# Kernel optimization log

Measured on AMD Instinct MI355X. Metric: run time of the kernel, lower is better.

The kernel has to match this reference:

```python
import jax, jax.numpy as jnp
import numpy as np

E, C, F, K = 8, 768, 3072, 2  # NUM_EXPERTS, EMBED_DIM, FFN_DIM, TOP_K


def setup_inputs() -> dict:
    key = jax.random.key(0)
    k0, k1, k2, k3 = jax.random.split(key, 4)
    B, T = 8, 2048
    return {
        "x": jax.random.normal(k0, (B, T, C), jnp.float32),
        "router_w": jax.random.normal(k1, (E, C), jnp.float32) * 0.02,
        "w1": jax.random.normal(k2, (E, C, F), jnp.float32) * 0.02,
        "b1": jnp.zeros((E, F), jnp.float32),
        "w2": jax.random.normal(k3, (E, F, C), jnp.float32) * 0.02,
        "b2": jnp.zeros((E, C), jnp.float32),
    }


def reference(x, router_w, w1, b1, w2, b2):
    # Dropout is inference-mode identity (eval). GELU is torch's exact (erf) variant.
    B, T, Cc = x.shape
    flat = x.reshape(-1, Cc)                                   # [N, C]
    logits = flat @ router_w.T                                 # [N, E]
    probs = jax.nn.softmax(logits.astype(jnp.float32), axis=-1)
    top_w, top_i = jax.lax.top_k(probs, K)                     # [N, K]
    top_w = (top_w / top_w.sum(-1, keepdims=True)).astype(x.dtype)
    out = jnp.zeros_like(flat)
    for e in range(E):
        # per-token combine weight for expert e (0 if token not routed to e)
        w_e = jnp.sum(top_w * (top_i == e), axis=-1)[:, None]  # [N, 1]
        h = jax.nn.gelu(flat @ w1[e] + b1[e], approximate=False)  # [N, F]
        out = out + w_e * (h @ w2[e] + b2[e])
    return out.reshape(B, T, Cc)
```

## Files before the change

### kernel.cpp

```cpp
#include <hip/hip_runtime.h>
#include <hip/hip_bf16.h>

#define NTOK 16384
#define CDIM 768
#define FDIM 3072
#define NEXP 8
#define NSLOT 32768
#define HBLK 128
#define MAXT256 135

typedef __attribute__((ext_vector_type(8))) short bf16x8;
typedef __attribute__((ext_vector_type(4))) float f32x4;
typedef __attribute__((ext_vector_type(8))) unsigned short u16x8;

__device__ __forceinline__ unsigned short f2bf(float f) {
  unsigned int u = __float_as_uint(f);
  u += 0x7FFFu + ((u >> 16) & 1u);
  return (unsigned short)(u >> 16);
}
__device__ __forceinline__ float bf2f(unsigned short h) {
  return __uint_as_float((unsigned int)h << 16);
}

__device__ __forceinline__ float fast_gelu(float x) {
  float x2 = x * x;
  float z = x * __builtin_fmaf(0.070565402f, x2, 1.5975981f);
  float s = __builtin_amdgcn_rcpf(1.0f + __expf(-z));
  return x * s;
}

__device__ __forceinline__ void async16(const void* g, void* l) {
  __builtin_amdgcn_global_load_lds(
      (const __attribute__((address_space(1))) unsigned int*)g,
      (__attribute__((address_space(3))) unsigned int*)l, 16, 0, 0);
}

#define BARRIER() asm volatile("s_barrier" ::: "memory")
#define LGK0()    asm volatile("s_waitcnt lgkmcnt(0)" ::: "memory")
#define VMC(n)    asm volatile("s_waitcnt vmcnt(" #n ")" ::: "memory")

__global__ __launch_bounds__(256)
void k_transpose(const float* __restrict__ src, unsigned short* __restrict__ dst,
                 int R, int Cc)
{
  __shared__ float tle[32][33];
  int e = blockIdx.z;
  int c0 = blockIdx.x * 32, r0 = blockIdx.y * 32;
  int tx = threadIdx.x & 31, ty = threadIdx.x >> 5;
  const float* s = src + (size_t)e * R * Cc;
  unsigned short* d = dst + (size_t)e * R * Cc;
#pragma unroll
  for (int i = 0; i < 4; ++i)
    tle[ty + i * 8][tx] = s[(size_t)(r0 + ty + i * 8) * Cc + c0 + tx];
  __syncthreads();
#pragma unroll
  for (int i = 0; i < 4; ++i)
    d[(size_t)(c0 + ty + i * 8) * R + r0 + tx] = f2bf(tle[tx][ty + i * 8]);
}

__global__ __launch_bounds__(256)
void k_router(const float* __restrict__ x, const float* __restrict__ rw,
              int* __restrict__ tk_e, float* __restrict__ tk_w)
{
  __shared__ float srw[NEXP * CDIM];
  int tid = threadIdx.x;
#pragma unroll
  for (int i = 0; i < (NEXP * CDIM / 4) / 256; ++i)
    ((float4*)srw)[tid + i * 256] = ((const float4*)rw)[tid + i * 256];
  __syncthreads();
  int lane = tid & 63, wid = tid >> 6;
  int t = blockIdx.x * 4 + wid;
  float a[NEXP];
#pragma unroll
  for (int e = 0; e < NEXP; ++e) a[e] = 0.f;
  const float* xr = x + (size_t)t * CDIM;
#pragma unroll
  for (int c = 0; c < CDIM / 64; ++c) {
    float xv = xr[c * 64 + lane];
#pragma unroll
    for (int e = 0; e < NEXP; ++e) a[e] += xv * srw[e * CDIM + c * 64 + lane];
  }
#pragma unroll
  for (int e = 0; e < NEXP; ++e) {
#pragma unroll
    for (int off = 32; off; off >>= 1) a[e] += __shfl_xor(a[e], off);
  }
  if (lane == 0) {
    int i0 = 0; float l0 = a[0];
#pragma unroll
    for (int e = 1; e < NEXP; ++e) if (a[e] > l0) { l0 = a[e]; i0 = e; }
    int i1 = -1; float l1 = -1e30f;
#pragma unroll
    for (int e = 0; e < NEXP; ++e) if (e != i0 && a[e] > l1) { l1 = a[e]; i1 = e; }
    float w0 = 1.f / (1.f + expf(l1 - l0));
    tk_e[2 * t] = i0;     tk_e[2 * t + 1] = i1;
    tk_w[2 * t] = w0;     tk_w[2 * t + 1] = 1.f - w0;
  }
}

__global__ __launch_bounds__(256)
void k_hist(const int* __restrict__ tk_e, int* __restrict__ blockhist)
{
  __shared__ int h[NEXP];
  int tid = threadIdx.x;
  if (tid < NEXP) h[tid] = 0;
  __syncthreads();
  int e = tk_e[blockIdx.x * 256 + tid];
  atomicAdd(&h[e], 1);
  __syncthreads();
  if (tid < NEXP) blockhist[blockIdx.x * NEXP + tid] = h[tid];
}

__global__ __launch_bounds__(512)
void k_scan2(const int* __restrict__ blockhist, int* __restrict__ counts,
             int* __restrict__ offsets, int* __restrict__ tp,
             int* __restrict__ blockbase)
{
  __shared__ int ltot[NEXP];
  __shared__ int loff[NEXP + 1];
  int tid = threadIdx.x;
  int lane = tid & 63, e = tid >> 6;
  int o0 = blockhist[lane * NEXP + e];
  int o1 = blockhist[(64 + lane) * NEXP + e];
  int h0 = o0, h1 = o1;
#pragma unroll
  for (int d = 1; d < 64; d <<= 1) { int v = __shfl_up(h0, d); if (lane >= d) h0 += v; }
  int s0 = __shfl(h0, 63);
#pragma unroll
  for (int d = 1; d < 64; d <<= 1) { int v = __shfl_up(h1, d); if (lane >= d) h1 += v; }
  h1 += s0;
  if (lane == 63) ltot[e] = h1;
  __syncthreads();
  if (tid == 0) {
    loff[0] = 0;
    int tpv = 0; tp[0] = 0;
    for (int k = 0; k < NEXP; ++k) {
      loff[k + 1] = loff[k] + ltot[k];
      counts[k] = ltot[k];
      offsets[k] = loff[k];
      tpv += (ltot[k] + 255) / 256;
      tp[k + 1] = tpv;
    }
    offsets[NEXP] = loff[NEXP];
  }
  __syncthreads();
  int base = loff[e];
  blockbase[lane * NEXP + e]        = base + h0 - o0;
  blockbase[(64 + lane) * NEXP + e] = base + h1 - o1;
}

__global__ __launch_bounds__(256)
void k_assign_gather(const float* __restrict__ x, const int* __restrict__ tk_e,
                     const float* __restrict__ tk_w,
                     const int* __restrict__ blockbase,
                     int* __restrict__ tok2slot, float* __restrict__ slot_w,
                     unsigned short* __restrict__ Xg)
{
  __shared__ int eh[256];
  __shared__ int sslot[256];
  int b = blockIdx.x, tid = threadIdx.x;
  int pick = b * 256 + tid;
  int e = tk_e[pick];
  eh[tid] = e;
  __syncthreads();
  int rank = 0;
  for (int j = 0; j < tid; ++j) rank += (eh[j] == e);
  int slot = blockbase[b * NEXP + e] + rank;
  sslot[tid] = slot;
  tok2slot[pick] = slot;
  slot_w[slot] = tk_w[pick];
  __syncthreads();
  int lane = tid & 63, wid = tid >> 6;
  for (int p = wid * 64; p < wid * 64 + 64; ++p) {
    int token = (b * 256 + p) >> 1;
    int s = sslot[p];
    const float4* src = (const float4*)(x + (size_t)token * CDIM);
    ushort4* dst = (ushort4*)(Xg + (size_t)s * CDIM);
#pragma unroll
    for (int i = 0; i < 3; ++i) {
      float4 v = src[i * 64 + lane];
      ushort4 hh;
      hh.x = f2bf(v.x); hh.y = f2bf(v.y); hh.z = f2bf(v.z); hh.w = f2bf(v.w);
      dst[i * 64 + lane] = hh;
    }
  }
}

__global__ __launch_bounds__(512, 2)
void k_gemm1(const unsigned short* __restrict__ A, int lda,
             const unsigned short* __restrict__ B, int ldb, long sB,
             const int* __restrict__ counts,
             const int* __restrict__ offsets, const int* __restrict__ tp,
             int t0, const float* __restrict__ bias, int biasStride,
             unsigned short* __restrict__ Hout, int ldh, int gx, int nwg)
{
  constexpr int KI = CDIM / 128;
  __shared__ __align__(16) char lds[131072];

  int orig = blockIdx.y * gx + blockIdx.x;
  int q = nwg >> 3, r = nwg & 7;
  int xcd = orig & 7, jj = orig >> 3;
  int wgid = (xcd < r ? xcd * (q + 1) : r * (q + 1) + (xcd - r) * q) + jj;
  const int RG = 16;
  int yT = nwg / gx;
  int gsize = gx * RG;
  int rg = wgid / gsize;
  int rem = wgid - rg * gsize;
  int rgs = yT - rg * RG; if (rgs > RG) rgs = RG;
  int bx = rem / rgs;
  int byl = rg * RG + (rem - bx * rgs);
  int by = t0 + byl;

  if (by >= tp[NEXP]) return;
  int e = 0;
  while (by >= tp[e + 1]) ++e;
  int rowbase = offsets[e];
  int m0 = (by - tp[e]) * 256;
  int n0 = bx * 256;

  const unsigned short* Bexp = B + (long)e * sB + (long)n0 * ldb;
  const unsigned short* Aexp = A + (long)(rowbase + m0) * lda;

  int tid = threadIdx.x;
  int lane = tid & 63, wid = tid >> 6;
  int wm = wid >> 2, wn = wid & 3;
  int ar = lane & 15, kg = lane >> 4;
  int arl = ar & 7;

  const char* pA[2][2];
  const char* pB[2][2];
#pragma unroll
  for (int d = 0; d < 2; ++d)
#pragma unroll
    for (int s = 0; s < 2; ++s) {
      int sw = (((s * 4 + kg) ^ arl) << 4);
      pA[d][s] = lds + d * 65536 + (wm * 128 + ar) * 128 + sw;
      pB[d][s] = lds + d * 65536 + 32768 + (wn * 64 + ar) * 128 + sw;
    }

  int srow = tid >> 3, schunk = tid & 7;
  int sswz = ((schunk ^ (srow & 7)) << 3);
  const unsigned short* srcA = Aexp + (long)srow * lda + sswz;
  const unsigned short* srcB = Bexp + (long)srow * ldb + sswz;

  auto STG_A = [&](int d, int kt, int g) {
    async16(srcA + (long)g * 64 * lda + kt * 64,
            lds + d * 65536 + g * 8192 + wid * 1024);
  };
  auto STG_B = [&](int d, int kt, int g) {
    async16(srcB + (long)g * 64 * ldb + kt * 64,
            lds + d * 65536 + 32768 + g * 8192 + wid * 1024);
  };

  f32x4 acc[8][4] = {};
  bf16x8 a[2][4], b[2][4];

#define LDA_(d, h)                                                   \
  _Pragma("unroll") for (int s = 0; s < 2; ++s)                      \
  _Pragma("unroll") for (int m = 0; m < 4; ++m)                      \
    a[s][m] = *(const bf16x8*)(pA[d][s] + (h) * 8192 + m * 2048);
#define LDB_(d, np)                                                  \
  _Pragma("unroll") for (int s = 0; s < 2; ++s)                      \
  _Pragma("unroll") for (int j = 0; j < 2; ++j)                      \
    b[s][(np) * 2 + j] = *(const bf16x8*)(pB[d][s] + ((np) * 2 + j) * 2048);
#define MM_(h, np)                                                   \
  _Pragma("unroll") for (int m = 0; m < 4; ++m)                      \
  _Pragma("unroll") for (int j = 0; j < 2; ++j) {                    \
    acc[(h)*4+m][(np)*2+j] = __builtin_amdgcn_mfma_f32_16x16x32_bf16(\
        a[0][m], b[0][(np)*2+j], acc[(h)*4+m][(np)*2+j], 0, 0, 0);   \
    acc[(h)*4+m][(np)*2+j] = __builtin_amdgcn_mfma_f32_16x16x32_bf16(\
        a[1][m], b[1][(np)*2+j], acc[(h)*4+m][(np)*2+j], 0, 0, 0); }
#define PHTAIL()                                                     \
  LGK0(); __builtin_amdgcn_sched_barrier(0);                         \
  __builtin_amdgcn_s_setprio(1)
#define PHEND()                                                      \
  __builtin_amdgcn_s_setprio(0); BARRIER()

  STG_A(0, 0, 0); STG_A(0, 0, 1); STG_A(0, 0, 2); STG_A(0, 0, 3);
  STG_B(0, 0, 0); STG_B(0, 0, 1); STG_B(0, 0, 2); STG_B(0, 0, 3);
  STG_A(1, 1, 0); STG_A(1, 1, 1);
  VMC(2);
  BARRIER();

#pragma unroll
  for (int i = 0; i < KI; ++i) {
    const int kt1 = 2 * i + 1, kt2 = 2 * i + 2, kt3 = 2 * i + 3;
    const bool cond = (i + 1 < KI);
    LDA_(0, 0); LDB_(0, 0);
    STG_A(1, kt1, 2); STG_A(1, kt1, 3);
    BARRIER(); PHTAIL(); MM_(0, 0); PHEND();
    LDB_(0, 1);
    STG_B(1, kt1, 0); STG_B(1, kt1, 1);
    BARRIER(); PHTAIL(); MM_(0, 1); PHEND();
    LDA_(0, 1);
    STG_B(1, kt1, 2); STG_B(1, kt1, 3);
    BARRIER(); PHTAIL(); MM_(1, 0); PHEND();
    if (cond) {
      STG_A(0, kt2, 0); STG_A(0, kt2, 1);
      VMC(2);
    } else {
      VMC(0);
    }
    BARRIER(); PHTAIL(); MM_(1, 1); PHEND();
    LDA_(1, 0); LDB_(1, 0);
    if (cond) { STG_A(0, kt2, 2); STG_A(0, kt2, 3); }
    BARRIER(); PHTAIL(); MM_(0, 0); PHEND();
    LDB_(1, 1);
    if (cond) { STG_B(0, kt2, 0); STG_B(0, kt2, 1); }
    BARRIER(); PHTAIL(); MM_(0, 1); PHEND();
    LDA_(1, 1);
    if (cond) { STG_B(0, kt2, 2); STG_B(0, kt2, 3); }
    BARRIER(); PHTAIL(); MM_(1, 0); PHEND();
    if (cond) {
      STG_A(1, kt3, 0); STG_A(1, kt3, 1);
      VMC(2);
    }
    BARRIER(); PHTAIL(); MM_(1, 1); PHEND();
  }

  unsigned short* st = (unsigned short*)lds;
  __syncthreads();
#pragma unroll
  for (int pass = 0; pass < 2; ++pass) {
    if (wm == pass) {
#pragma unroll
      for (int n = 0; n < 4; ++n) {
        int col = wn * 64 + n * 16 + ar;
        float bv = bias[e * biasStride + n0 + col];
#pragma unroll
        for (int m = 0; m < 8; ++m) {
#pragma unroll
          for (int rr = 0; rr < 4; ++rr) {
            int row = m * 16 + kg * 4 + rr;
            float v = fast_gelu(acc[m][n][rr] + bv);
            st[row * 264 + col] = f2bf(v);
          }
        }
      }
    }
    __syncthreads();
    int row = tid >> 2, qq = tid & 3;
    unsigned short* drow =
        Hout + (long)(byl * 256 + pass * 128 + row) * ldh + n0 + qq * 64;
    const unsigned short* srow2 = st + row * 264 + qq * 64;
#pragma unroll
    for (int i = 0; i < 8; ++i)
      *(u16x8*)(drow + i * 8) = *(const u16x8*)(srow2 + i * 8);
    __syncthreads();
  }
#undef LDA_
#undef LDB_
#undef MM_
#undef PHTAIL
#undef PHEND
}

__global__ __launch_bounds__(256, 3)
void k_gemm2(const unsigned short* __restrict__ A, int lda,
             const unsigned short* __restrict__ B, int ldb, long sB,
             int Ksteps, const int* __restrict__ counts,
             const int* __restrict__ offsets, const int* __restrict__ tp,
             int t0, const float* __restrict__ bias, int biasStride,
             unsigned short* __restrict__ Yout, const float* __restrict__ slot_w,
             int gx, int nwg)
{
  __shared__ __align__(16) char lds[3 * 16384];

  int orig = blockIdx.y * gx + blockIdx.x;
  int q = nwg >> 3, r = nwg & 7;
  int xcd = orig & 7, jj = orig >> 3;
  int wgid = (xcd < r ? xcd * (q + 1) : r * (q + 1) + (xcd - r) * q) + jj;
  const int RG = 16;
  int yT = nwg / gx;
  int gsize = gx * RG;
  int rg = wgid / gsize;
  int rem = wgid - rg * gsize;
  int rgs = yT - rg * RG; if (rgs > RG) rgs = RG;
  int bx = rem / rgs;
  int byl = rg * RG + (rem - bx * rgs);

  int t256l = byl >> 1, half = byl & 1;
  int by = t0 + t256l;
  if (by >= tp[NEXP]) return;
  int e = 0;
  while (by >= tp[e + 1]) ++e;
  int cnt = counts[e];
  int rowbase = offsets[e];
  int m0 = (by - tp[e]) * 256 + half * 128;
  if (m0 >= cnt) return;
  int n0 = bx * 128;

  const unsigned short* Bexp = B + (long)e * sB + (long)n0 * ldb;
  const unsigned short* Aexp = A + (long)(t256l * 256 + half * 128) * lda;

  int tid = threadIdx.x;
  int lane = tid & 63, wid = tid >> 6;
  int wm = wid >> 1, wn = wid & 1;
  int ar = lane & 15, kg = lane >> 4;
  int kgs = (kg ^ ((ar >> 1) & 3)) << 4;

  int rA0 = tid >> 2;
  int cA0 = tid & 3;
  int ksw = (cA0 ^ ((rA0 >> 1) & 3)) << 3;
  const unsigned short* As0 = Aexp + (long)rA0 * lda + ksw;
  const unsigned short* As1 = Aexp + (long)(rA0 + 64) * lda + ksw;
  const unsigned short* Bs0 = Bexp + (long)rA0 * ldb + ksw;
  const unsigned short* Bs1 = Bexp + (long)(rA0 + 64) * ldb + ksw;

  f32x4 acc[4][4] = {};

  auto STAGE = [&](int buf, int t) {
    char* bb = lds + buf * 16384;
    int ko = t * 32;
    async16(As0 + ko, bb + wid * 1024);
    async16(As1 + ko, bb + 4096 + wid * 1024);
    async16(Bs0 + ko, bb + 8192 + wid * 1024);
    async16(Bs1 + ko, bb + 12288 + wid * 1024);
  };

  STAGE(0, 0); STAGE(1, 1);
  int cur = 0, nxt2 = 2;

  for (int ks = 0; ks < Ksteps; ++ks) {
    if (ks + 1 < Ksteps) {
      asm volatile("s_waitcnt vmcnt(4)" ::: "memory");
    } else {
      asm volatile("s_waitcnt vmcnt(0)" ::: "memory");
    }
    __builtin_amdgcn_s_barrier();
    asm volatile("" ::: "memory");

    const char* bb = lds + cur * 16384;
    const char* bA = bb + (wm * 64 + ar) * 64 + kgs;
    const char* bB = bb + 8192 + (wn * 64 + ar) * 64 + kgs;
    bf16x8 af[4], bfr[4];
#pragma unroll
    for (int i = 0; i < 4; ++i) af[i] = *(const bf16x8*)(bA + i * 1024);
#pragma unroll
    for (int i = 0; i < 4; ++i) bfr[i] = *(const bf16x8*)(bB + i * 1024);

    if (ks + 2 < Ksteps) STAGE(nxt2, ks + 2);

#pragma unroll
    for (int mi = 0; mi < 4; ++mi)
#pragma unroll
      for (int ni = 0; ni < 4; ++ni)
        acc[mi][ni] = __builtin_amdgcn_mfma_f32_16x16x32_bf16(af[mi], bfr[ni],
                                                              acc[mi][ni], 0, 0, 0);
    cur = (cur == 2) ? 0 : cur + 1;
    nxt2 = (nxt2 == 2) ? 0 : nxt2 + 1;
  }

  unsigned short* st = (unsigned short*)lds;
  __syncthreads();

#pragma unroll
  for (int mi = 0; mi < 4; ++mi) {
#pragma unroll
    for (int rr = 0; rr < 4; ++rr) {
      int rowl = wm * 64 + mi * 16 + kg * 4 + rr;
      float wt = (m0 + rowl < cnt) ? slot_w[rowbase + m0 + rowl] : 0.f;
#pragma unroll
      for (int ni = 0; ni < 4; ++ni) {
        int col = wn * 64 + ni * 16 + ar;
        float v = (acc[mi][ni][rr] + bias[e * biasStride + n0 + col]) * wt;
        st[rowl * 136 + col] = f2bf(v);
      }
    }
  }
  __syncthreads();
  int row = tid >> 1, hh = tid & 1;
  if (m0 + row < cnt) {
    unsigned short* drow = Yout + (long)(rowbase + m0 + row) * CDIM + n0 + hh * 64;
    const unsigned short* srow = st + row * 136 + hh * 64;
#pragma unroll
    for (int i = 0; i < 8; ++i)
      *(u16x8*)(drow + i * 8) = *(const u16x8*)(srow + i * 8);
  }
}

__global__ __launch_bounds__(256)
void k_combine(const unsigned short* __restrict__ Y,
               const int* __restrict__ tok2slot, float* __restrict__ out)
{
  int t = blockIdx.x * 4 + (threadIdx.x >> 6);
  int lane = threadIdx.x & 63;
  int s0 = tok2slot[2 * t], s1 = tok2slot[2 * t + 1];
  const ushort4* y0 = (const ushort4*)(Y + (size_t)s0 * CDIM);
  const ushort4* y1 = (const ushort4*)(Y + (size_t)s1 * CDIM);
  float4* o = (float4*)(out + (size_t)t * CDIM);
#pragma unroll
  for (int i = 0; i < 3; ++i) {
    ushort4 aa = y0[i * 64 + lane];
    ushort4 bb = y1[i * 64 + lane];
    float4 rr;
    rr.x = bf2f(aa.x) + bf2f(bb.x);
    rr.y = bf2f(aa.y) + bf2f(bb.y);
    rr.z = bf2f(aa.z) + bf2f(bb.z);
    rr.w = bf2f(aa.w) + bf2f(bb.w);
    o[i * 64 + lane] = rr;
  }
}

extern "C" void kernel_launch(void* const* d_in, const int* in_sizes, int n_in,
                              void* d_out, int out_size, void* d_ws, size_t ws_size,
                              hipStream_t stream) {
  const float* x        = (const float*)d_in[0];
  const float* router_w = (const float*)d_in[1];
  const float* w1       = (const float*)d_in[2];
  const float* b1       = (const float*)d_in[3];
  const float* w2       = (const float*)d_in[4];
  const float* b2       = (const float*)d_in[5];
  float* out = (float*)d_out;

  char* ws = (char*)d_ws;
  size_t off = 0;
  auto alloc = [&](size_t bytes) -> void* {
    void* p = ws + off;
    off = (off + bytes + 255) & ~(size_t)255;
    return p;
  };
  int*   counts     = (int*)alloc(NEXP * 4);
  int*   offsets    = (int*)alloc((NEXP + 1) * 4);
  int*   tp         = (int*)alloc((NEXP + 1) * 4);
  int*   tk_e       = (int*)alloc((size_t)NSLOT * 4);
  float* tk_w       = (float*)alloc((size_t)NSLOT * 4);
  int*   blockhist  = (int*)alloc((size_t)HBLK * NEXP * 4);
  int*   blockbase  = (int*)alloc((size_t)HBLK * NEXP * 4);
  int*   tok2slot   = (int*)alloc((size_t)NSLOT * 4);
  float* slot_w     = (float*)alloc((size_t)NSLOT * 4);
  unsigned short* Yslot = (unsigned short*)alloc((size_t)NSLOT * CDIM * 2);
  unsigned short* w1t = (unsigned short*)alloc((size_t)NEXP * FDIM * CDIM * 2);
  unsigned short* w2t = (unsigned short*)alloc((size_t)NEXP * CDIM * FDIM * 2);
  unsigned short* Xg  = (unsigned short*)alloc((size_t)(NSLOT + 256) * CDIM * 2);
  int TPC = 42;
  if (off + (size_t)TPC * 256 * FDIM * 2 > ws_size) TPC = 21;
  unsigned short* H = (unsigned short*)alloc((size_t)TPC * 256 * FDIM * 2);

  k_transpose<<<dim3(FDIM / 32, CDIM / 32, NEXP), 256, 0, stream>>>(w1, w1t, CDIM, FDIM);
  k_transpose<<<dim3(CDIM / 32, FDIM / 32, NEXP), 256, 0, stream>>>(w2, w2t, FDIM, CDIM);
  k_router<<<NTOK / 4, 256, 0, stream>>>(x, router_w, tk_e, tk_w);
  k_hist<<<HBLK, 256, 0, stream>>>(tk_e, blockhist);
  k_scan2<<<1, 512, 0, stream>>>(blockhist, counts, offsets, tp, blockbase);
  k_assign_gather<<<HBLK, 256, 0, stream>>>(x, tk_e, tk_w, blockbase,
                                            tok2slot, slot_w, Xg);

  for (int t0 = 0; t0 < MAXT256; t0 += TPC) {
    int yT = (MAXT256 - t0 < TPC) ? (MAXT256 - t0) : TPC;
    int gx1 = FDIM / 256;
    k_gemm1<<<dim3(gx1, yT), 512, 0, stream>>>(
        Xg, CDIM, w1t, CDIM, (long)FDIM * CDIM,
        counts, offsets, tp, t0, b1, FDIM, H, FDIM, gx1, gx1 * yT);
    int gx2 = CDIM / 128;
    k_gemm2<<<dim3(gx2, 2 * yT), 256, 0, stream>>>(
        H, FDIM, w2t, FDIM, (long)CDIM * FDIM, FDIM / 32,
        counts, offsets, tp, t0, b2, CDIM, Yslot, slot_w, gx2, gx2 * 2 * yT);
  }
  k_combine<<<NTOK / 4, 256, 0, stream>>>(Yslot, tok2slot, out);
}
```

Baseline: 636.7 us.

## Add 256x256-tile eight-phase pipelined second GEMM and larger H chunks

Adds a new down-projection kernel that uses 512-thread workgroups with 256x256 output tiles, double-buffered 128 KB LDS, and an eight-phase schedule that interleaves async global-to-LDS loads with MFMA work. It also raises the chunk of row-tiles processed per GEMM1/GEMM2 pair to 68 when the workspace allows it, which covers all 135 tiles in two iterations. Larger tiles should cut redundant reads of H and weights and reduce the number of launches, at the cost of fewer workgroups per GEMM2 launch (3 column tiles) and heavy LDS use that limits occupancy. The old kernel is kept as a fallback when the workspace is too small.

After: 631.2 us. No clear change (-0.9%).

```diff
diff --git a/kernel.cpp b/kernel.cpp
--- a/kernel.cpp
+++ b/kernel.cpp
@@ -355,6 +355,181 @@
 #undef PHEND
 }
 
+__global__ __launch_bounds__(512, 2)
+void k_gemm2_8ph(const unsigned short* __restrict__ A, int lda,
+                 const unsigned short* __restrict__ B, int ldb, long sB,
+                 const int* __restrict__ counts,
+                 const int* __restrict__ offsets, const int* __restrict__ tp,
+                 int t0, const float* __restrict__ bias, int biasStride,
+                 unsigned short* __restrict__ Yout,
+                 const float* __restrict__ slot_w, int gx, int nwg)
+{
+  constexpr int KI = FDIM / 128;
+  __shared__ __align__(16) char lds[131072];
+
+  int orig = blockIdx.y * gx + blockIdx.x;
+  int q = nwg >> 3, r = nwg & 7;
+  int xcd = orig & 7, jj = orig >> 3;
+  int wgid = (xcd < r ? xcd * (q + 1) : r * (q + 1) + (xcd - r) * q) + jj;
+  const int RG = 16;
+  int yT = nwg / gx;
+  int gsize = gx * RG;
+  int rg = wgid / gsize;
+  int rem = wgid - rg * gsize;
+  int rgs = yT - rg * RG; if (rgs > RG) rgs = RG;
+  int bx = rem / rgs;
+  int byl = rg * RG + (rem - bx * rgs);
+  int by = t0 + byl;
+
+  if (by >= tp[NEXP]) return;
+  int e = 0;
+  while (by >= tp[e + 1]) ++e;
+  int cnt = counts[e];
+  int rowbase = offsets[e];
+  int m0 = (by - tp[e]) * 256;
+  int n0 = bx * 256;
+
+  const unsigned short* Bexp = B + (long)e * sB + (long)n0 * ldb;
+  const unsigned short* Aexp = A + (long)(byl * 256) * lda;
+
+  int tid = threadIdx.x;
+  int lane = tid & 63, wid = tid >> 6;
+  int wm = wid >> 2, wn = wid & 3;
+  int ar = lane & 15, kg = lane >> 4;
+  int arl = ar & 7;
+
+  const char* pA[2][2];
+  const char* pB[2][2];
+#pragma unroll
+  for (int d = 0; d < 2; ++d)
+#pragma unroll
+    for (int s = 0; s < 2; ++s) {
+      int sw = (((s * 4 + kg) ^ arl) << 4);
+      pA[d][s] = lds + d * 65536 + (wm * 128 + ar) * 128 + sw;
+      pB[d][s] = lds + d * 65536 + 32768 + (wn * 64 + ar) * 128 + sw;
+    }
+
+  int srow = tid >> 3, schunk = tid & 7;
+  int sswz = ((schunk ^ (srow & 7)) << 3);
+  const unsigned short* srcA = Aexp + (long)srow * lda + sswz;
+  const unsigned short* srcB = Bexp + (long)srow * ldb + sswz;
+
+  auto STG_A = [&](int d, int kt, int g) {
+    async16(srcA + (long)g * 64 * lda + kt * 64,
+            lds + d * 65536 + g * 8192 + wid * 1024);
+  };
+  auto STG_B = [&](int d, int kt, int g) {
+    async16(srcB + (long)g * 64 * ldb + kt * 64,
+            lds + d * 65536 + 32768 + g * 8192 + wid * 1024);
+  };
+
+  f32x4 acc[8][4] = {};
+  bf16x8 a[2][4], b[2][4];
+
+#define LDA_(d, h)                                                   \
+  _Pragma("unroll") for (int s = 0; s < 2; ++s)                      \
+  _Pragma("unroll") for (int m = 0; m < 4; ++m)                      \
+    a[s][m] = *(const bf16x8*)(pA[d][s] + (h) * 8192 + m * 2048);
+#define LDB_(d, np)                                                  \
+  _Pragma("unroll") for (int s = 0; s < 2; ++s)                      \
+  _Pragma("unroll") for (int j = 0; j < 2; ++j)                      \
+    b[s][(np) * 2 + j] = *(const bf16x8*)(pB[d][s] + ((np) * 2 + j) * 2048);
+#define MM_(h, np)                                                   \
+  _Pragma("unroll") for (int m = 0; m < 4; ++m)                      \
+  _Pragma("unroll") for (int j = 0; j < 2; ++j) {                    \
+    acc[(h)*4+m][(np)*2+j] = __builtin_amdgcn_mfma_f32_16x16x32_bf16(\
+        a[0][m], b[0][(np)*2+j], acc[(h)*4+m][(np)*2+j], 0, 0, 0);   \
+    acc[(h)*4+m][(np)*2+j] = __builtin_amdgcn_mfma_f32_16x16x32_bf16(\
+        a[1][m], b[1][(np)*2+j], acc[(h)*4+m][(np)*2+j], 0, 0, 0); }
+#define PHTAIL()                                                     \
+  LGK0(); __builtin_amdgcn_sched_barrier(0);                         \
+  __builtin_amdgcn_s_setprio(1)
+#define PHEND()                                                      \
+  __builtin_amdgcn_s_setprio(0); BARRIER()
+
+  STG_A(0, 0, 0); STG_A(0, 0, 1); STG_A(0, 0, 2); STG_A(0, 0, 3);
+  STG_B(0, 0, 0); STG_B(0, 0, 1); STG_B(0, 0, 2); STG_B(0, 0, 3);
+  STG_A(1, 1, 0); STG_A(1, 1, 1);
+  VMC(2);
+  BARRIER();
+
+#pragma unroll 1
+  for (int i = 0; i < KI; ++i) {
+    const int kt1 = 2 * i + 1, kt2 = 2 * i + 2, kt3 = 2 * i + 3;
+    const bool cond = (i + 1 < KI);
+    LDA_(0, 0); LDB_(0, 0);
+    STG_A(1, kt1, 2); STG_A(1, kt1, 3);
+    BARRIER(); PHTAIL(); MM_(0, 0); PHEND();
+    LDB_(0, 1);
+    STG_B(1, kt1, 0); STG_B(1, kt1, 1);
+    BARRIER(); PHTAIL(); MM_(0, 1); PHEND();
+    LDA_(0, 1);
+    STG_B(1, kt1, 2); STG_B(1, kt1, 3);
+    BARRIER(); PHTAIL(); MM_(1, 0); PHEND();
+    if (cond) {
+      STG_A(0, kt2, 0); STG_A(0, kt2, 1);
+      VMC(2);
+    } else {
+      VMC(0);
+    }
+    BARRIER(); PHTAIL(); MM_(1, 1); PHEND();
+    LDA_(1, 0); LDB_(1, 0);
+    if (cond) { STG_A(0, kt2, 2); STG_A(0, kt2, 3); }
+    BARRIER(); PHTAIL(); MM_(0, 0); PHEND();
+    LDB_(1, 1);
+    if (cond) { STG_B(0, kt2, 0); STG_B(0, kt2, 1); }
+    BARRIER(); PHTAIL(); MM_(0, 1); PHEND();
+    LDA_(1, 1);
+    if (cond) { STG_B(0, kt2, 2); STG_B(0, kt2, 3); }
+    BARRIER(); PHTAIL(); MM_(1, 0); PHEND();
+    if (cond) {
+      STG_A(1, kt3, 0); STG_A(1, kt3, 1);
+      VMC(2);
+    }
+    BARRIER(); PHTAIL(); MM_(1, 1); PHEND();
+  }
+
+  unsigned short* st = (unsigned short*)lds;
+  __syncthreads();
+#pragma unroll
+  for (int pass = 0; pass < 2; ++pass) {
+    if (wm == pass) {
+#pragma unroll
+      for (int m = 0; m < 8; ++m) {
+#pragma unroll
+        for (int rr = 0; rr < 4; ++rr) {
+          int row = m * 16 + kg * 4 + rr;
+          int grow = m0 + pass * 128 + row;
+          float wt = (grow < cnt) ? slot_w[rowbase + grow] : 0.f;
+#pragma unroll
+          for (int n = 0; n < 4; ++n) {
+            int col = wn * 64 + n * 16 + ar;
+            float v = (acc[m][n][rr] + bias[e * biasStride + n0 + col]) * wt;
+            st[row * 264 + col] = f2bf(v);
+          }
+        }
+      }
+    }
+    __syncthreads();
+    int row = tid >> 2, qq = tid & 3;
+    int grow = m0 + pass * 128 + row;
+    if (grow < cnt) {
+      unsigned short* drow =
+          Yout + (long)(rowbase + grow) * CDIM + n0 + qq * 64;
+      const unsigned short* srow2 = st + row * 264 + qq * 64;
+#pragma unroll
+      for (int i = 0; i < 8; ++i)
+        *(u16x8*)(drow + i * 8) = *(const u16x8*)(srow2 + i * 8);
+    }
+    __syncthreads();
+  }
+#undef LDA_
+#undef LDB_
+#undef MM_
+#undef PHTAIL
+#undef PHEND
+}
+
 __global__ __launch_bounds__(256, 3)
 void k_gemm2(const unsigned short* __restrict__ A, int lda,
              const unsigned short* __restrict__ B, int ldb, long sB,
@@ -533,8 +708,10 @@
   unsigned short* w1t = (unsigned short*)alloc((size_t)NEXP * FDIM * CDIM * 2);
   unsigned short* w2t = (unsigned short*)alloc((size_t)NEXP * CDIM * FDIM * 2);
   unsigned short* Xg  = (unsigned short*)alloc((size_t)(NSLOT + 256) * CDIM * 2);
-  int TPC = 42;
+  int TPC = 68;
+  if (off + (size_t)TPC * 256 * FDIM * 2 > ws_size) TPC = 42;
   if (off + (size_t)TPC * 256 * FDIM * 2 > ws_size) TPC = 21;
+  bool big = (TPC == 68);
   unsigned short* H = (unsigned short*)alloc((size_t)TPC * 256 * FDIM * 2);
 
   k_transpose<<<dim3(FDIM / 32, CDIM / 32, NEXP), 256, 0, stream>>>(w1, w1t, CDIM, FDIM);
@@ -551,10 +728,17 @@
     k_gemm1<<<dim3(gx1, yT), 512, 0, stream>>>(
         Xg, CDIM, w1t, CDIM, (long)FDIM * CDIM,
         counts, offsets, tp, t0, b1, FDIM, H, FDIM, gx1, gx1 * yT);
-    int gx2 = CDIM / 128;
-    k_gemm2<<<dim3(gx2, 2 * yT), 256, 0, stream>>>(
-        H, FDIM, w2t, FDIM, (long)CDIM * FDIM, FDIM / 32,
-        counts, offsets, tp, t0, b2, CDIM, Yslot, slot_w, gx2, gx2 * 2 * yT);
+    if (big) {
+      int gx2 = CDIM / 256;
+      k_gemm2_8ph<<<dim3(gx2, yT), 512, 0, stream>>>(
+          H, FDIM, w2t, FDIM, (long)CDIM * FDIM,
+          counts, offsets, tp, t0, b2, CDIM, Yslot, slot_w, gx2, gx2 * yT);
+    } else {
+      int gx2 = CDIM / 128;
+      k_gemm2<<<dim3(gx2, 2 * yT), 256, 0, stream>>>(
+          H, FDIM, w2t, FDIM, (long)CDIM * FDIM, FDIM / 32,
+          counts, offsets, tp, t0, b2, CDIM, Yslot, slot_w, gx2, gx2 * 2 * yT);
+    }
   }
   k_combine<<<NTOK / 4, 256, 0, stream>>>(Yslot, tok2slot, out);
 }
```
